# Kernel tuning notes

Hardware: AMD Instinct MI355X
Metric: run time of the kernel (lower is better)

The kernel has to match this reference:

```python
import jax, jax.numpy as jnp
import numpy as np

B, H, W = 2, 56, 56
D_MODEL, D_STATE, D_CONV, DT_RANK, K = 96, 16, 3, 6, 4
D_INNER = 192  # expand=2.0 * d_model


def _hscan1(x):
    # torch get_horizontal_scan1: flip odd columns along H; involution. x: (B,C,H,W)
    cols = (jnp.arange(x.shape[3]) % 2) == 1
    return jnp.where(cols[None, None, None, :], x[:, :, ::-1, :], x)


def _vscan1(x):
    # torch get_vertical_scan1: flip odd rows along W, then transpose H<->W. (B,C,H,W)->(B,C,W,H)
    rows = (jnp.arange(x.shape[2]) % 2) == 1
    x = jnp.where(rows[None, None, :, None], x[:, :, :, ::-1], x)
    return jnp.swapaxes(x, 2, 3)


def _revert_vscan1(x):
    # inverse of _vscan1. x: (B,C,W,H) -> (B,C,H,W)
    x = jnp.swapaxes(x, 2, 3)
    rows = (jnp.arange(x.shape[2]) % 2) == 1
    return jnp.where(rows[None, None, :, None], x[:, :, :, ::-1], x)


def _selective_scan(u, delta, A, Bs, Cs, D, delta_bias):
    # u, delta: (B, K*d, L); A: (K*d, N); Bs, Cs: (B, K, N, L); D: (K*d,)
    Bb, KD, L = u.shape
    k = Bs.shape[1]
    d = KD // k
    N = A.shape[1]
    delta = jax.nn.softplus(delta + delta_bias[None, :, None])
    u4 = u.reshape(Bb, k, d, L)
    dt4 = delta.reshape(Bb, k, d, L)
    A4 = A.reshape(k, d, N)
    dA = jnp.exp(jnp.einsum('bkdl,kdn->lbkdn', dt4, A4))           # (L,B,K,d,N)
    dBu = jnp.einsum('bkdl,bknl,bkdl->lbkdn', dt4, Bs, u4)          # (L,B,K,d,N)
    Ct = jnp.transpose(Cs, (3, 0, 1, 2))                            # (L,B,K,N)
    h0 = jnp.zeros((Bb, k, d, N), u.dtype)

    def step(h, inp):
        dA_t, dBu_t, C_t = inp
        h = dA_t * h + dBu_t
        y = jnp.einsum('bkdn,bkn->bkd', h, C_t)
        return h, y

    _, ys = jax.lax.scan(step, h0, (dA, dBu, Ct))                   # ys: (L,B,K,d)
    y = jnp.transpose(ys, (1, 2, 3, 0)).reshape(Bb, KD, L)
    return y + u * D[None, :, None]


def reference(x, in_proj_w, conv_w, conv_b, x_proj_weight, dt_projs_weight,
              dt_projs_bias, A_logs, Ds, out_norm_w, out_norm_b, out_proj_w):
    Bb, Hh, Ww, _ = x.shape
    L = Hh * Ww
    xz = jnp.einsum('bhwc,ec->bhwe', x, in_proj_w)
    xc, z = jnp.split(xz, 2, axis=-1)
    xc = jnp.transpose(xc, (0, 3, 1, 2))                            # (B, d_inner, H, W)
    xc = jax.lax.conv_general_dilated(xc, conv_w, (1, 1), ((1, 1), (1, 1)),
                                      feature_group_count=D_INNER)
    xc = jax.nn.silu(xc + conv_b[None, :, None, None])
    # torch code mutates x in place: vertical scan sees the h-scanned tensor
    x1 = _hscan1(xc)
    x_hw = x1.reshape(Bb, 1, D_INNER, L)
    x2 = _vscan1(x1)
    x_wh = x2.reshape(Bb, 1, D_INNER, L)
    xs = jnp.concatenate([x_hw, x_wh, x_hw[..., ::-1], x_wh[..., ::-1]], axis=1)  # (B,K,d,L)
    x_dbl = jnp.einsum('bkdl,kcd->bkcl', xs, x_proj_weight)
    dts, Bs, Cs = jnp.split(x_dbl, [DT_RANK, DT_RANK + D_STATE], axis=2)
    dts = jnp.einsum('bkrl,kdr->bkdl', dts, dt_projs_weight)
    u = xs.reshape(Bb, K * D_INNER, L)
    delta = dts.reshape(Bb, K * D_INNER, L)
    A = -jnp.exp(A_logs)
    out_y = _selective_scan(u, delta, A, Bs, Cs, Ds, dt_projs_bias.reshape(-1))
    oy = out_y.reshape(Bb, K, D_INNER, L)
    # revert scans back to a common spatial layout and sum
    s0 = _hscan1(oy[:, 0].reshape(Bb, D_INNER, Hh, Ww))
    s2 = _hscan1(oy[:, 2, :, ::-1].reshape(Bb, D_INNER, Hh, Ww))
    s1 = _hscan1(_revert_vscan1(oy[:, 1].reshape(Bb, D_INNER, Ww, Hh)))
    s3 = _hscan1(_revert_vscan1(oy[:, 3, :, ::-1].reshape(Bb, D_INNER, Ww, Hh)))
    y = (s0 + s1 + s2 + s3).reshape(Bb, D_INNER, L)
    y = jnp.transpose(y, (0, 2, 1))                                 # (B, L, d_inner)
    mu = jnp.mean(y, axis=-1, keepdims=True)
    var = jnp.var(y, axis=-1, keepdims=True)
    y = (y - mu) / jnp.sqrt(var + 1e-5) * out_norm_w + out_norm_b
    y = y.reshape(Bb, Hh, Ww, D_INNER) * jax.nn.silu(z)
    return jnp.einsum('bhwd,cd->bhwc', y, out_proj_w)


def setup_inputs():
    key = jax.random.key(0)
    ks = jax.random.split(key, 8)
    s = 0.02
    return {
        "x": jax.random.normal(ks[0], (B, H, W, D_MODEL), jnp.float32),
        "in_proj_w": jax.random.normal(ks[1], (2 * D_INNER, D_MODEL), jnp.float32) * s,
        "conv_w": jax.random.normal(ks[2], (D_INNER, 1, D_CONV, D_CONV), jnp.float32) * s,
        "conv_b": jnp.zeros((D_INNER,), jnp.float32),
        "x_proj_weight": jax.random.normal(ks[3], (K, DT_RANK + 2 * D_STATE, D_INNER), jnp.float32) * s,
        "dt_projs_weight": jax.random.normal(ks[4], (K, D_INNER, DT_RANK), jnp.float32) * (DT_RANK ** -0.5),
        "dt_projs_bias": jax.random.uniform(ks[5], (K, D_INNER), jnp.float32, -4.6, -2.3),
        "A_logs": jnp.log(jnp.tile(jnp.arange(1, D_STATE + 1, dtype=jnp.float32)[None, :], (K * D_INNER, 1))),
        "Ds": jnp.ones((K * D_INNER,), jnp.float32),
        "out_norm_w": jnp.ones((D_INNER,), jnp.float32),
        "out_norm_b": jnp.zeros((D_INNER,), jnp.float32),
        "out_proj_w": jax.random.normal(ks[6], (D_MODEL, D_INNER), jnp.float32) * s,
    }
```

## Files before the change

kernel.cpp:

```cpp
#include <hip/hip_runtime.h>
#include <hip/hip_bf16.h>

#define BB 2
#define HH 56
#define WW 56
#define LL (HH*WW)
#define DM 96
#define DI 192
#define NS 16
#define DTR 6
#define KK 4
#define CDBL (DTR + 2*NS)
#define CS 32
#define NC 98
#define ROWS (BB*KK*DI)

#define IP_BM 32
__global__ __launch_bounds__(256) void k_inproj(const float* __restrict__ x,
                                                const float* __restrict__ w,
                                                float* __restrict__ xcpre,
                                                float* __restrict__ zsilu) {
    __shared__ float xl[IP_BM*100];
    __shared__ float wl[64*100];
    int t = threadIdx.x;
    int bl0 = blockIdx.x * IP_BM;
    for (int idx = t; idx < IP_BM*96; idx += 256) {
        int r = idx/96, c = idx%96;
        xl[r*100+c] = x[(bl0+r)*DM + c];
    }
    int pg = t >> 4, eg = t & 15;
    for (int nc = 0; nc < 6; ++nc) {
        __syncthreads();
        for (int idx = t; idx < 64*96; idx += 256) {
            int r = idx/96, c = idx%96;
            wl[r*100+c] = w[(nc*64+r)*DM + c];
        }
        __syncthreads();
        float acc[2][4] = {};
        #pragma unroll 4
        for (int k = 0; k < 96; ++k) {
            float a0 = xl[(pg*2+0)*100+k];
            float a1 = xl[(pg*2+1)*100+k];
            float b0 = wl[(eg*4+0)*100+k];
            float b1 = wl[(eg*4+1)*100+k];
            float b2 = wl[(eg*4+2)*100+k];
            float b3 = wl[(eg*4+3)*100+k];
            acc[0][0] = fmaf(a0,b0,acc[0][0]); acc[0][1] = fmaf(a0,b1,acc[0][1]);
            acc[0][2] = fmaf(a0,b2,acc[0][2]); acc[0][3] = fmaf(a0,b3,acc[0][3]);
            acc[1][0] = fmaf(a1,b0,acc[1][0]); acc[1][1] = fmaf(a1,b1,acc[1][1]);
            acc[1][2] = fmaf(a1,b2,acc[1][2]); acc[1][3] = fmaf(a1,b3,acc[1][3]);
        }
        #pragma unroll
        for (int j = 0; j < 2; ++j) {
            int bl = bl0 + pg*2 + j;
            #pragma unroll
            for (int jj = 0; jj < 4; ++jj) {
                int e = nc*64 + eg*4 + jj;
                float v = acc[j][jj];
                if (e < DI) xcpre[(size_t)bl*DI + e] = v;
                else        zsilu[(size_t)bl*DI + (e-DI)] = v / (1.f + expf(-v));
            }
        }
    }
}

__global__ __launch_bounds__(DI) void k_conv(const float* __restrict__ xcpre,
                                             const float* __restrict__ cw,
                                             const float* __restrict__ cb,
                                             float* __restrict__ xs0,
                                             float* __restrict__ xs1) {
    int bl = blockIdx.x;
    int b = bl / LL, l = bl % LL;
    int h = l / WW, w = l % WW;
    int c = threadIdx.x;
    float acc = cb[c];
    #pragma unroll
    for (int dh = -1; dh <= 1; ++dh) {
        int hh = h + dh;
        if (hh < 0 || hh >= HH) continue;
        #pragma unroll
        for (int dw = -1; dw <= 1; ++dw) {
            int ww2 = w + dw;
            if (ww2 < 0 || ww2 >= WW) continue;
            acc = fmaf(xcpre[(b*LL + hh*WW + ww2)*DI + c],
                       cw[c*9 + (dh+1)*3 + (dw+1)], acc);
        }
    }
    float v = acc / (1.f + expf(-acc));
    int i  = (w & 1) ? (HH-1-h) : h;
    int l0 = i*WW + w;
    int l1 = ((i & 1) ? (WW-1-w) : w)*HH + i;
    xs0[(b*LL + l0)*DI + c] = v;
    xs1[(b*LL + l1)*DI + c] = v;
}

#define TL 32
#define KCH 48
#define NKC 4
#define XSTR 52
#define WSTR 52
__global__ __launch_bounds__(256) void k_proj(const float* __restrict__ xs0,
                                              const float* __restrict__ xs1,
                                              const float* __restrict__ xpw,
                                              const float* __restrict__ dtw,
                                              const float* __restrict__ dtb,
                                              float* __restrict__ delta,
                                              float* __restrict__ Bsb,
                                              float* __restrict__ Csb) {
    int tile = blockIdx.x, k = blockIdx.y, b = blockIdx.z;
    int bk = b*KK + k;
    int t = threadIdx.x;
    __shared__ float Xl[TL*XSTR];
    __shared__ float Wl[39*WSTR];
    __shared__ float dblL[DTR*36];

    const float* src = (k & 1) ? xs1 : xs0;
    const bool rev = (k >= 2);
    int cp = t >> 4, lp = t & 15;

    float acc[3][2] = {};
    for (int kc = 0; kc < NKC; ++kc) {
        __syncthreads();
        for (int idx = t; idx < 39*12; idx += 256) {
            int r = idx/12, q = idx%12;
            float4 v = (r < CDBL)
                ? ((const float4*)(xpw + (size_t)k*CDBL*DI + (size_t)r*DI + kc*KCH))[q]
                : make_float4(0.f,0.f,0.f,0.f);
            *(float4*)&Wl[r*WSTR + 4*q] = v;
        }
        for (int idx = t; idx < TL*12; idx += 256) {
            int ll = idx/12, q = idx%12;
            int lg = tile*TL + ll;
            int lpos = rev ? (LL-1-lg) : lg;
            *(float4*)&Xl[ll*XSTR + 4*q] =
                ((const float4*)(src + (size_t)(b*LL + lpos)*DI + kc*KCH))[q];
        }
        __syncthreads();
        if (cp < 13) {
            const float4* w0 = (const float4*)&Wl[(3*cp+0)*WSTR];
            const float4* w1 = (const float4*)&Wl[(3*cp+1)*WSTR];
            const float4* w2 = (const float4*)&Wl[(3*cp+2)*WSTR];
            const float4* x0 = (const float4*)&Xl[(lp    )*XSTR];
            const float4* x1 = (const float4*)&Xl[(lp+16)*XSTR];
            #pragma unroll
            for (int q = 0; q < 12; ++q) {
                float4 wa = w0[q], wb = w1[q], wc = w2[q];
                float4 xa = x0[q], xb = x1[q];
                acc[0][0]=fmaf(wa.x,xa.x,acc[0][0]); acc[0][0]=fmaf(wa.y,xa.y,acc[0][0]);
                acc[0][0]=fmaf(wa.z,xa.z,acc[0][0]); acc[0][0]=fmaf(wa.w,xa.w,acc[0][0]);
                acc[0][1]=fmaf(wa.x,xb.x,acc[0][1]); acc[0][1]=fmaf(wa.y,xb.y,acc[0][1]);
                acc[0][1]=fmaf(wa.z,xb.z,acc[0][1]); acc[0][1]=fmaf(wa.w,xb.w,acc[0][1]);
                acc[1][0]=fmaf(wb.x,xa.x,acc[1][0]); acc[1][0]=fmaf(wb.y,xa.y,acc[1][0]);
                acc[1][0]=fmaf(wb.z,xa.z,acc[1][0]); acc[1][0]=fmaf(wb.w,xa.w,acc[1][0]);
                acc[1][1]=fmaf(wb.x,xb.x,acc[1][1]); acc[1][1]=fmaf(wb.y,xb.y,acc[1][1]);
                acc[1][1]=fmaf(wb.z,xb.z,acc[1][1]); acc[1][1]=fmaf(wb.w,xb.w,acc[1][1]);
                acc[2][0]=fmaf(wc.x,xa.x,acc[2][0]); acc[2][0]=fmaf(wc.y,xa.y,acc[2][0]);
                acc[2][0]=fmaf(wc.z,xa.z,acc[2][0]); acc[2][0]=fmaf(wc.w,xa.w,acc[2][0]);
                acc[2][1]=fmaf(wc.x,xb.x,acc[2][1]); acc[2][1]=fmaf(wc.y,xb.y,acc[2][1]);
                acc[2][1]=fmaf(wc.z,xb.z,acc[2][1]); acc[2][1]=fmaf(wc.w,xb.w,acc[2][1]);
            }
        }
    }
    if (cp < 13) {
        #pragma unroll
        for (int ci = 0; ci < 3; ++ci) {
            int c = 3*cp + ci;
            if (c < CDBL) {
                #pragma unroll
                for (int li = 0; li < 2; ++li) {
                    int ll = lp + 16*li;
                    int lg = tile*TL + ll;
                    float v = acc[ci][li];
                    if (c < DTR)          dblL[c*36 + ll] = v;
                    else if (c < DTR+NS)  Bsb[((size_t)bk*LL + lg)*NS + (c-DTR)] = v;
                    else                  Csb[((size_t)bk*LL + lg)*NS + (c-DTR-NS)] = v;
                }
            }
        }
    }
    __syncthreads();

    float wr0[DTR], wr1[DTR], wr2[DTR], bb0, bb1, bb2;
    {
        int d0 = t % DI, d1 = (t+64) % DI, d2 = (t+128) % DI;
        #pragma unroll
        for (int r = 0; r < DTR; ++r) {
            wr0[r] = dtw[((size_t)k*DI + d0)*DTR + r];
            wr1[r] = dtw[((size_t)k*DI + d1)*DTR + r];
            wr2[r] = dtw[((size_t)k*DI + d2)*DTR + r];
        }
        bb0 = dtb[k*DI + d0]; bb1 = dtb[k*DI + d1]; bb2 = dtb[k*DI + d2];
    }
    float* dbase = delta + ((size_t)bk*LL + (size_t)tile*TL)*DI;
    for (int j3 = 0; j3 < 8; ++j3) {
        #pragma unroll
        for (int jj = 0; jj < 3; ++jj) {
            int j = j3*3 + jj;
            int idx = t + 256*j;
            int d = idx % DI;
            int ll = idx / DI;
            float a = (jj == 0) ? bb0 : (jj == 1) ? bb1 : bb2;
            const float* wrp = (jj == 0) ? wr0 : (jj == 1) ? wr1 : wr2;
            #pragma unroll
            for (int r = 0; r < DTR; ++r) a = fmaf(wrp[r], dblL[r*36 + ll], a);
            float sp = fmaxf(a, 0.f) + log1pf(expf(-fabsf(a)));
            dbase[(size_t)ll*DI + d] = sp;
        }
    }
}

__global__ __launch_bounds__(192) void k_scan1(const float* __restrict__ delta,
                                               const float* __restrict__ xs0,
                                               const float* __restrict__ xs1,
                                               const float* __restrict__ Bsb,
                                               const float* __restrict__ A_logs,
                                               float* __restrict__ P,
                                               float* __restrict__ Hend) {
    int c = blockIdx.x, bk = blockIdx.y;
    int k = bk & 3, b = bk >> 2;
    int d = threadIdx.x;
    int kd = k*DI + d;
    __shared__ float Bl[CS*NS];
    const float* bsrc = Bsb + ((size_t)bk*LL + c*CS)*NS;
    for (int i = threadIdx.x; i < CS*NS/4; i += 192)
        ((float4*)Bl)[i] = ((const float4*)bsrc)[i];

    float A[NS], h[NS], p[NS];
    #pragma unroll
    for (int q = 0; q < 4; ++q) {
        float4 av = *(const float4*)&A_logs[kd*NS + 4*q];
        A[4*q+0] = -expf(av.x); A[4*q+1] = -expf(av.y);
        A[4*q+2] = -expf(av.z); A[4*q+3] = -expf(av.w);
    }
    #pragma unroll
    for (int n = 0; n < NS; ++n) { h[n] = 0.f; p[n] = 1.f; }
    __syncthreads();

    const bool rev = (k >= 2);
    const float* dp = delta + ((size_t)bk*LL + c*CS)*DI + d;
    const float* up = ((k & 1) ? xs1 : xs0) + (size_t)b*LL*DI + d;
    const int l0 = c*CS;

    #pragma unroll 2
    for (int i = 0; i < CS; ++i) {
        float dt = dp[(size_t)i*DI];
        int lp = rev ? (LL-1-(l0+i)) : (l0+i);
        float u = up[(size_t)lp*DI];
        float dtu = dt * u;
        float Bv[NS];
        #pragma unroll
        for (int q = 0; q < 4; ++q)
            *(float4*)&Bv[4*q] = *(const float4*)&Bl[i*NS + 4*q];
        #pragma unroll
        for (int n = 0; n < NS; ++n) {
            float dA = __expf(dt * A[n]);
            h[n] = fmaf(dA, h[n], dtu * Bv[n]);
            p[n] *= dA;
        }
    }
    size_t obase = ((size_t)c*ROWS + bk*DI + d)*NS;
    #pragma unroll
    for (int q = 0; q < 4; ++q) {
        *(float4*)&P[obase + 4*q]    = make_float4(p[4*q], p[4*q+1], p[4*q+2], p[4*q+3]);
        *(float4*)&Hend[obase + 4*q] = make_float4(h[4*q], h[4*q+1], h[4*q+2], h[4*q+3]);
    }
}

__global__ __launch_bounds__(256) void k_scanmid(const float* __restrict__ P,
                                                 const float* __restrict__ Hend,
                                                 float* __restrict__ Hin) {
    int tid = blockIdx.x*256 + threadIdx.x;
    float h = 0.f;
    for (int c = 0; c < NC; ++c) {
        size_t idx = (size_t)c*(ROWS*NS) + tid;
        Hin[idx] = h;
        h = fmaf(P[idx], h, Hend[idx]);
    }
}

__global__ __launch_bounds__(192) void k_scan2(const float* __restrict__ delta,
                                               const float* __restrict__ xs0,
                                               const float* __restrict__ xs1,
                                               const float* __restrict__ Bsb,
                                               const float* __restrict__ Csb,
                                               const float* __restrict__ A_logs,
                                               const float* __restrict__ Ds,
                                               const float* __restrict__ Hin,
                                               float* __restrict__ oy) {
    int c = blockIdx.x, bk = blockIdx.y;
    int k = bk & 3, b = bk >> 2;
    int d = threadIdx.x;
    int kd = k*DI + d;
    __shared__ float Bl[CS*NS];
    __shared__ float Cl[CS*NS];
    const float* bsrc = Bsb + ((size_t)bk*LL + c*CS)*NS;
    const float* csrc = Csb + ((size_t)bk*LL + c*CS)*NS;
    for (int i = threadIdx.x; i < CS*NS/4; i += 192) {
        ((float4*)Bl)[i] = ((const float4*)bsrc)[i];
        ((float4*)Cl)[i] = ((const float4*)csrc)[i];
    }

    float A[NS], h[NS];
    #pragma unroll
    for (int q = 0; q < 4; ++q) {
        float4 av = *(const float4*)&A_logs[kd*NS + 4*q];
        A[4*q+0] = -expf(av.x); A[4*q+1] = -expf(av.y);
        A[4*q+2] = -expf(av.z); A[4*q+3] = -expf(av.w);
    }
    size_t ibase = ((size_t)c*ROWS + bk*DI + d)*NS;
    #pragma unroll
    for (int q = 0; q < 4; ++q) {
        float4 hv = *(const float4*)&Hin[ibase + 4*q];
        h[4*q+0] = hv.x; h[4*q+1] = hv.y; h[4*q+2] = hv.z; h[4*q+3] = hv.w;
    }
    const float Dv = Ds[kd];
    __syncthreads();

    const bool rev = (k >= 2);
    const float* dp = delta + ((size_t)bk*LL + c*CS)*DI + d;
    const float* up = ((k & 1) ? xs1 : xs0) + (size_t)b*LL*DI + d;
    float* yp = oy + ((size_t)bk*LL + c*CS)*DI + d;
    const int l0 = c*CS;

    #pragma unroll 2
    for (int i = 0; i < CS; ++i) {
        float dt = dp[(size_t)i*DI];
        int lp = rev ? (LL-1-(l0+i)) : (l0+i);
        float u = up[(size_t)lp*DI];
        float dtu = dt * u;
        float Bv[NS], Cv[NS];
        #pragma unroll
        for (int q = 0; q < 4; ++q) {
            *(float4*)&Bv[4*q] = *(const float4*)&Bl[i*NS + 4*q];
            *(float4*)&Cv[4*q] = *(const float4*)&Cl[i*NS + 4*q];
        }
        float acc = 0.f;
        #pragma unroll
        for (int n = 0; n < NS; ++n) {
            float dA = __expf(dt * A[n]);
            h[n] = fmaf(dA, h[n], dtu * Bv[n]);
            acc = fmaf(h[n], Cv[n], acc);
        }
        yp[(size_t)i*DI] = fmaf(u, Dv, acc);
    }
}

#define OP_BM 32
__global__ __launch_bounds__(256) void k_out(const float* __restrict__ oy,
                                             const float* __restrict__ zsilu,
                                             const float* __restrict__ onw,
                                             const float* __restrict__ onb,
                                             const float* __restrict__ opw,
                                             float* __restrict__ out) {
    __shared__ float yv[OP_BM*196];
    __shared__ float wl[96*68];
    int t = threadIdx.x;
    int bl0 = blockIdx.x * OP_BM;
    int lane = t & 63, wv = t >> 6;

    for (int pp = 0; pp < 8; ++pp) {
        int p = wv*8 + pp;
        int bl = bl0 + p;
        int b = bl / LL, l = bl % LL;
        int h = l / WW, w2 = l % WW;
        int i = (w2 & 1) ? (HH-1-h) : h;
        int l0 = i*WW + w2;
        int l1 = ((i & 1) ? (WW-1-w2) : w2)*HH + i;
        size_t base = (size_t)b*KK*LL*DI;
        float yd[3]; float s1 = 0.f, s2 = 0.f;
        #pragma unroll
        for (int j = 0; j < 3; ++j) {
            int c = lane + j*64;
            float v = oy[base + (size_t)(0*LL + l0)*DI + c]
                    + oy[base + (size_t)(1*LL + l1)*DI + c]
                    + oy[base + (size_t)(2*LL + (LL-1-l0))*DI + c]
                    + oy[base + (size_t)(3*LL + (LL-1-l1))*DI + c];
            yd[j] = v; s1 += v; s2 += v*v;
        }
        #pragma unroll
        for (int m = 1; m < 64; m <<= 1) { s1 += __shfl_xor(s1, m); s2 += __shfl_xor(s2, m); }
        float mu  = s1 / DI;
        float var = s2 / DI - mu*mu;
        float ry  = rsqrtf(var + 1e-5f);
        #pragma unroll
        for (int j = 0; j < 3; ++j) {
            int c = lane + j*64;
            float yn = (yd[j] - mu) * ry * onw[c] + onb[c];
            yv[p*196 + c] = yn * zsilu[(size_t)bl*DI + c];
        }
    }

    int pg = t >> 5, eg = t & 31;
    float acc[4][3] = {};
    for (int kc = 0; kc < 3; ++kc) {
        __syncthreads();
        for (int idx = t; idx < 96*64; idx += 256) {
            int r = idx >> 6, c = idx & 63;
            wl[r*68 + c] = opw[r*DI + kc*64 + c];
        }
        __syncthreads();
        #pragma unroll 4
        for (int kk = 0; kk < 64; ++kk) {
            float a[4], bq[3];
            #pragma unroll
            for (int j = 0; j < 4; ++j)  a[j]  = yv[(pg*4+j)*196 + kc*64 + kk];
            #pragma unroll
            for (int jj = 0; jj < 3; ++jj) bq[jj] = wl[(eg*3+jj)*68 + kk];
            #pragma unroll
            for (int j = 0; j < 4; ++j)
                #pragma unroll
                for (int jj = 0; jj < 3; ++jj)
                    acc[j][jj] = fmaf(a[j], bq[jj], acc[j][jj]);
        }
    }
    #pragma unroll
    for (int j = 0; j < 4; ++j) {
        int bl = bl0 + pg*4 + j;
        #pragma unroll
        for (int jj = 0; jj < 3; ++jj)
            out[(size_t)bl*DM + eg*3 + jj] = acc[j][jj];
    }
}

extern "C" void kernel_launch(void* const* d_in, const int* in_sizes, int n_in,
                              void* d_out, int out_size, void* d_ws, size_t ws_size,
                              hipStream_t stream) {
    const float* x      = (const float*)d_in[0];
    const float* ipw    = (const float*)d_in[1];
    const float* convw  = (const float*)d_in[2];
    const float* convb  = (const float*)d_in[3];
    const float* xpw    = (const float*)d_in[4];
    const float* dtw    = (const float*)d_in[5];
    const float* dtb    = (const float*)d_in[6];
    const float* A_logs = (const float*)d_in[7];
    const float* Ds     = (const float*)d_in[8];
    const float* onw    = (const float*)d_in[9];
    const float* onb    = (const float*)d_in[10];
    const float* opw    = (const float*)d_in[11];
    float* out = (float*)d_out;

    float* ws = (float*)d_ws;
    const size_t SZ_BLD  = (size_t)BB*LL*DI;
    const size_t SZ_BKLD = (size_t)BB*KK*LL*DI;
    const size_t SZ_BKLN = (size_t)BB*KK*LL*NS;
    const size_t SZ_ST   = (size_t)NC*ROWS*NS;
    float* xcpre = ws;
    float* zsilu = xcpre + SZ_BLD;
    float* xs0   = zsilu + SZ_BLD;
    float* xs1   = xs0   + SZ_BLD;
    float* delta = xs1   + SZ_BLD;
    float* Bsb   = delta + SZ_BKLD;
    float* Csb   = Bsb   + SZ_BKLN;
    float* oy    = Csb   + SZ_BKLN;
    float* Hin   = oy    + SZ_BKLD;
    float* Hend  = oy;
    float* P     = oy + SZ_ST;

    k_inproj<<<(BB*LL)/IP_BM, 256, 0, stream>>>(x, ipw, xcpre, zsilu);
    k_conv<<<BB*LL, DI, 0, stream>>>(xcpre, convw, convb, xs0, xs1);
    dim3 g3(LL/TL, KK, BB);
    k_proj<<<g3, 256, 0, stream>>>(xs0, xs1, xpw, dtw, dtb, delta, Bsb, Csb);
    dim3 gs(NC, BB*KK);
    k_scan1<<<gs, 192, 0, stream>>>(delta, xs0, xs1, Bsb, A_logs, P, Hend);
    k_scanmid<<<(ROWS*NS)/256, 256, 0, stream>>>(P, Hend, Hin);
    k_scan2<<<gs, 192, 0, stream>>>(delta, xs0, xs1, Bsb, Csb, A_logs, Ds, Hin, oy);
    k_out<<<(BB*LL)/OP_BM, 256, 0, stream>>>(oy, zsilu, onw, onb, opw, out);
}
```

Measured before the change: 259.1 us.

## Vectorize shared-memory GEMM loads, flatten conv indexing, restructure delta softplus

The in_proj and out_proj GEMM inner loops now read float4 vectors from LDS, and the in_proj weight rows are permuted so each thread reads contiguous rows. Global-to-LDS staging uses float4 loads without per-element div/mod. The depthwise conv uses a 3D grid with explicit neighbour offsets and fast __expf. In k_proj, each of 192 threads now computes delta for one channel across all 32 positions, using fast exp/log intrinsics. Together these aim to cut integer index arithmetic and LDS instruction count, at some cost in accuracy from the fast math and extra register pressure in the delta loop.

```diff
diff --git a/kernel.cpp b/kernel.cpp
--- a/kernel.cpp
+++ b/kernel.cpp
@@ -24,31 +24,45 @@
     __shared__ float wl[64*100];
     int t = threadIdx.x;
     int bl0 = blockIdx.x * IP_BM;
-    for (int idx = t; idx < IP_BM*96; idx += 256) {
-        int r = idx/96, c = idx%96;
-        xl[r*100+c] = x[(bl0+r)*DM + c];
-    }
+    int qs = t & 31;
+    for (int r = t >> 5; r < IP_BM; r += 8)
+        if (qs < 24)
+            *(float4*)&xl[r*100 + 4*qs] = *(const float4*)&x[(size_t)(bl0+r)*DM + 4*qs];
     int pg = t >> 4, eg = t & 15;
     for (int nc = 0; nc < 6; ++nc) {
         __syncthreads();
-        for (int idx = t; idx < 64*96; idx += 256) {
-            int r = idx/96, c = idx%96;
-            wl[r*100+c] = w[(nc*64+r)*DM + c];
-        }
+        for (int r = t >> 5; r < 64; r += 8)
+            if (qs < 24)
+                *(float4*)&wl[((r&3)*16 + (r>>2))*100 + 4*qs] =
+                    *(const float4*)&w[(size_t)(nc*64+r)*DM + 4*qs];
         __syncthreads();
         float acc[2][4] = {};
-        #pragma unroll 4
-        for (int k = 0; k < 96; ++k) {
-            float a0 = xl[(pg*2+0)*100+k];
-            float a1 = xl[(pg*2+1)*100+k];
-            float b0 = wl[(eg*4+0)*100+k];
-            float b1 = wl[(eg*4+1)*100+k];
-            float b2 = wl[(eg*4+2)*100+k];
-            float b3 = wl[(eg*4+3)*100+k];
-            acc[0][0] = fmaf(a0,b0,acc[0][0]); acc[0][1] = fmaf(a0,b1,acc[0][1]);
-            acc[0][2] = fmaf(a0,b2,acc[0][2]); acc[0][3] = fmaf(a0,b3,acc[0][3]);
-            acc[1][0] = fmaf(a1,b0,acc[1][0]); acc[1][1] = fmaf(a1,b1,acc[1][1]);
-            acc[1][2] = fmaf(a1,b2,acc[1][2]); acc[1][3] = fmaf(a1,b3,acc[1][3]);
+        const float4* xa4 = (const float4*)&xl[(pg*2+0)*100];
+        const float4* xb4 = (const float4*)&xl[(pg*2+1)*100];
+        const float4* w0 = (const float4*)&wl[(0*16+eg)*100];
+        const float4* w1 = (const float4*)&wl[(1*16+eg)*100];
+        const float4* w2 = (const float4*)&wl[(2*16+eg)*100];
+        const float4* w3 = (const float4*)&wl[(3*16+eg)*100];
+        #pragma unroll 6
+        for (int q = 0; q < 24; ++q) {
+            float4 xa = xa4[q], xb = xb4[q];
+            float4 b0 = w0[q], b1 = w1[q], b2 = w2[q], b3 = w3[q];
+            acc[0][0]=fmaf(xa.x,b0.x,acc[0][0]); acc[0][0]=fmaf(xa.y,b0.y,acc[0][0]);
+            acc[0][0]=fmaf(xa.z,b0.z,acc[0][0]); acc[0][0]=fmaf(xa.w,b0.w,acc[0][0]);
+            acc[0][1]=fmaf(xa.x,b1.x,acc[0][1]); acc[0][1]=fmaf(xa.y,b1.y,acc[0][1]);
+            acc[0][1]=fmaf(xa.z,b1.z,acc[0][1]); acc[0][1]=fmaf(xa.w,b1.w,acc[0][1]);
+            acc[0][2]=fmaf(xa.x,b2.x,acc[0][2]); acc[0][2]=fmaf(xa.y,b2.y,acc[0][2]);
+            acc[0][2]=fmaf(xa.z,b2.z,acc[0][2]); acc[0][2]=fmaf(xa.w,b2.w,acc[0][2]);
+            acc[0][3]=fmaf(xa.x,b3.x,acc[0][3]); acc[0][3]=fmaf(xa.y,b3.y,acc[0][3]);
+            acc[0][3]=fmaf(xa.z,b3.z,acc[0][3]); acc[0][3]=fmaf(xa.w,b3.w,acc[0][3]);
+            acc[1][0]=fmaf(xb.x,b0.x,acc[1][0]); acc[1][0]=fmaf(xb.y,b0.y,acc[1][0]);
+            acc[1][0]=fmaf(xb.z,b0.z,acc[1][0]); acc[1][0]=fmaf(xb.w,b0.w,acc[1][0]);
+            acc[1][1]=fmaf(xb.x,b1.x,acc[1][1]); acc[1][1]=fmaf(xb.y,b1.y,acc[1][1]);
+            acc[1][1]=fmaf(xb.z,b1.z,acc[1][1]); acc[1][1]=fmaf(xb.w,b1.w,acc[1][1]);
+            acc[1][2]=fmaf(xb.x,b2.x,acc[1][2]); acc[1][2]=fmaf(xb.y,b2.y,acc[1][2]);
+            acc[1][2]=fmaf(xb.z,b2.z,acc[1][2]); acc[1][2]=fmaf(xb.w,b2.w,acc[1][2]);
+            acc[1][3]=fmaf(xb.x,b3.x,acc[1][3]); acc[1][3]=fmaf(xb.y,b3.y,acc[1][3]);
+            acc[1][3]=fmaf(xb.z,b3.z,acc[1][3]); acc[1][3]=fmaf(xb.w,b3.w,acc[1][3]);
         }
         #pragma unroll
         for (int j = 0; j < 2; ++j) {
@@ -58,7 +72,7 @@
                 int e = nc*64 + eg*4 + jj;
                 float v = acc[j][jj];
                 if (e < DI) xcpre[(size_t)bl*DI + e] = v;
-                else        zsilu[(size_t)bl*DI + (e-DI)] = v / (1.f + expf(-v));
+                else        zsilu[(size_t)bl*DI + (e-DI)] = v / (1.f + __expf(-v));
             }
         }
     }
@@ -69,36 +83,38 @@
                                              const float* __restrict__ cb,
                                              float* __restrict__ xs0,
                                              float* __restrict__ xs1) {
-    int bl = blockIdx.x;
-    int b = bl / LL, l = bl % LL;
-    int h = l / WW, w = l % WW;
+    int w = blockIdx.x, h = blockIdx.y, b = blockIdx.z;
     int c = threadIdx.x;
+    const float* src = xcpre + ((size_t)(b*LL + h*WW + w))*DI + c;
+    const float* cwc = cw + c*9;
     float acc = cb[c];
-    #pragma unroll
-    for (int dh = -1; dh <= 1; ++dh) {
-        int hh = h + dh;
-        if (hh < 0 || hh >= HH) continue;
-        #pragma unroll
-        for (int dw = -1; dw <= 1; ++dw) {
-            int ww2 = w + dw;
-            if (ww2 < 0 || ww2 >= WW) continue;
-            acc = fmaf(xcpre[(b*LL + hh*WW + ww2)*DI + c],
-                       cw[c*9 + (dh+1)*3 + (dw+1)], acc);
-        }
-    }
-    float v = acc / (1.f + expf(-acc));
+    if (h > 0) {
+        if (w > 0)      acc = fmaf(src[-(WW+1)*DI], cwc[0], acc);
+                        acc = fmaf(src[-WW*DI],     cwc[1], acc);
+        if (w < WW-1)   acc = fmaf(src[-(WW-1)*DI], cwc[2], acc);
+    }
+    {
+        if (w > 0)      acc = fmaf(src[-DI],        cwc[3], acc);
+                        acc = fmaf(src[0],          cwc[4], acc);
+        if (w < WW-1)   acc = fmaf(src[DI],         cwc[5], acc);
+    }
+    if (h < HH-1) {
+        if (w > 0)      acc = fmaf(src[(WW-1)*DI],  cwc[6], acc);
+                        acc = fmaf(src[WW*DI],      cwc[7], acc);
+        if (w < WW-1)   acc = fmaf(src[(WW+1)*DI],  cwc[8], acc);
+    }
+    float v = acc / (1.f + __expf(-acc));
     int i  = (w & 1) ? (HH-1-h) : h;
     int l0 = i*WW + w;
     int l1 = ((i & 1) ? (WW-1-w) : w)*HH + i;
-    xs0[(b*LL + l0)*DI + c] = v;
-    xs1[(b*LL + l1)*DI + c] = v;
+    xs0[((size_t)b*LL + l0)*DI + c] = v;
+    xs1[((size_t)b*LL + l1)*DI + c] = v;
 }
 
 #define TL 32
 #define KCH 48
 #define NKC 4
-#define XSTR 52
-#define WSTR 52
+#define LSTR 52
 __global__ __launch_bounds__(256) void k_proj(const float* __restrict__ xs0,
                                               const float* __restrict__ xs1,
                                               const float* __restrict__ xpw,
@@ -110,38 +126,39 @@
     int tile = blockIdx.x, k = blockIdx.y, b = blockIdx.z;
     int bk = b*KK + k;
     int t = threadIdx.x;
-    __shared__ float Xl[TL*XSTR];
-    __shared__ float Wl[39*WSTR];
+    __shared__ float Xl[TL*LSTR];
+    __shared__ float Wl[39*LSTR];
     __shared__ float dblL[DTR*36];
 
     const float* src = (k & 1) ? xs1 : xs0;
     const bool rev = (k >= 2);
     int cp = t >> 4, lp = t & 15;
+    int qs = t & 15;
 
     float acc[3][2] = {};
     for (int kc = 0; kc < NKC; ++kc) {
         __syncthreads();
-        for (int idx = t; idx < 39*12; idx += 256) {
-            int r = idx/12, q = idx%12;
-            float4 v = (r < CDBL)
-                ? ((const float4*)(xpw + (size_t)k*CDBL*DI + (size_t)r*DI + kc*KCH))[q]
-                : make_float4(0.f,0.f,0.f,0.f);
-            *(float4*)&Wl[r*WSTR + 4*q] = v;
-        }
-        for (int idx = t; idx < TL*12; idx += 256) {
-            int ll = idx/12, q = idx%12;
-            int lg = tile*TL + ll;
-            int lpos = rev ? (LL-1-lg) : lg;
-            *(float4*)&Xl[ll*XSTR + 4*q] =
-                ((const float4*)(src + (size_t)(b*LL + lpos)*DI + kc*KCH))[q];
-        }
+        for (int r = t >> 4; r < 39; r += 16)
+            if (qs < 12) {
+                float4 v = (r < CDBL)
+                    ? *(const float4*)&xpw[(size_t)k*CDBL*DI + (size_t)r*DI + kc*KCH + 4*qs]
+                    : make_float4(0.f,0.f,0.f,0.f);
+                *(float4*)&Wl[r*LSTR + 4*qs] = v;
+            }
+        for (int r = t >> 4; r < TL; r += 16)
+            if (qs < 12) {
+                int lg = tile*TL + r;
+                int lpos = rev ? (LL-1-lg) : lg;
+                *(float4*)&Xl[r*LSTR + 4*qs] =
+                    *(const float4*)&src[(size_t)(b*LL + lpos)*DI + kc*KCH + 4*qs];
+            }
         __syncthreads();
         if (cp < 13) {
-            const float4* w0 = (const float4*)&Wl[(3*cp+0)*WSTR];
-            const float4* w1 = (const float4*)&Wl[(3*cp+1)*WSTR];
-            const float4* w2 = (const float4*)&Wl[(3*cp+2)*WSTR];
-            const float4* x0 = (const float4*)&Xl[(lp    )*XSTR];
-            const float4* x1 = (const float4*)&Xl[(lp+16)*XSTR];
+            const float4* w0 = (const float4*)&Wl[(3*cp+0)*LSTR];
+            const float4* w1 = (const float4*)&Wl[(3*cp+1)*LSTR];
+            const float4* w2 = (const float4*)&Wl[(3*cp+2)*LSTR];
+            const float4* x0 = (const float4*)&Xl[(lp    )*LSTR];
+            const float4* x1 = (const float4*)&Xl[(lp+16)*LSTR];
             #pragma unroll
             for (int q = 0; q < 12; ++q) {
                 float4 wa = w0[q], wb = w1[q], wc = w2[q];
@@ -180,31 +197,34 @@
     }
     __syncthreads();
 
-    float wr0[DTR], wr1[DTR], wr2[DTR], bb0, bb1, bb2;
-    {
-        int d0 = t % DI, d1 = (t+64) % DI, d2 = (t+128) % DI;
+    if (t < DI) {
+        int d = t;
+        float wr[DTR];
+        #pragma unroll
+        for (int r = 0; r < DTR; ++r) wr[r] = dtw[((size_t)k*DI + d)*DTR + r];
+        float bias = dtb[k*DI + d];
+        float a2[TL];
+        #pragma unroll
+        for (int ll = 0; ll < TL; ++ll) a2[ll] = bias;
         #pragma unroll
         for (int r = 0; r < DTR; ++r) {
-            wr0[r] = dtw[((size_t)k*DI + d0)*DTR + r];
-            wr1[r] = dtw[((size_t)k*DI + d1)*DTR + r];
-            wr2[r] = dtw[((size_t)k*DI + d2)*DTR + r];
-        }
-        bb0 = dtb[k*DI + d0]; bb1 = dtb[k*DI + d1]; bb2 = dtb[k*DI + d2];
-    }
-    float* dbase = delta + ((size_t)bk*LL + (size_t)tile*TL)*DI;
-    for (int j3 = 0; j3 < 8; ++j3) {
-        #pragma unroll
-        for (int jj = 0; jj < 3; ++jj) {
-            int j = j3*3 + jj;
-            int idx = t + 256*j;
-            int d = idx % DI;
-            int ll = idx / DI;
-            float a = (jj == 0) ? bb0 : (jj == 1) ? bb1 : bb2;
-            const float* wrp = (jj == 0) ? wr0 : (jj == 1) ? wr1 : wr2;
+            float wv = wr[r];
+            const float4* db = (const float4*)&dblL[r*36];
             #pragma unroll
-            for (int r = 0; r < DTR; ++r) a = fmaf(wrp[r], dblL[r*36 + ll], a);
-            float sp = fmaxf(a, 0.f) + log1pf(expf(-fabsf(a)));
-            dbase[(size_t)ll*DI + d] = sp;
+            for (int q = 0; q < 8; ++q) {
+                float4 v = db[q];
+                a2[4*q+0] = fmaf(wv, v.x, a2[4*q+0]);
+                a2[4*q+1] = fmaf(wv, v.y, a2[4*q+1]);
+                a2[4*q+2] = fmaf(wv, v.z, a2[4*q+2]);
+                a2[4*q+3] = fmaf(wv, v.w, a2[4*q+3]);
+            }
+        }
+        float* dst = delta + ((size_t)bk*LL + (size_t)tile*TL)*DI + d;
+        #pragma unroll
+        for (int ll = 0; ll < TL; ++ll) {
+            float a = a2[ll];
+            float sp = fmaxf(a, 0.f) + __logf(1.f + __expf(-fabsf(a)));
+            dst[ll*DI] = sp;
         }
     }
 }
@@ -356,12 +376,13 @@
     __shared__ float wl[96*68];
     int t = threadIdx.x;
     int bl0 = blockIdx.x * OP_BM;
+    int b = (blockIdx.x >= (LL/OP_BM)) ? 1 : 0;
+    int lbase = bl0 - b*LL;
     int lane = t & 63, wv = t >> 6;
 
     for (int pp = 0; pp < 8; ++pp) {
         int p = wv*8 + pp;
-        int bl = bl0 + p;
-        int b = bl / LL, l = bl % LL;
+        int l = lbase + p;
         int h = l / WW, w2 = l % WW;
         int i = (w2 & 1) ? (HH-1-h) : h;
         int l0 = i*WW + w2;
@@ -386,7 +407,7 @@
         for (int j = 0; j < 3; ++j) {
             int c = lane + j*64;
             float yn = (yd[j] - mu) * ry * onw[c] + onb[c];
-            yv[p*196 + c] = yn * zsilu[(size_t)bl*DI + c];
+            yv[p*196 + c] = yn * zsilu[(size_t)(bl0+p)*DI + c];
         }
     }
 
@@ -394,23 +415,45 @@
     float acc[4][3] = {};
     for (int kc = 0; kc < 3; ++kc) {
         __syncthreads();
-        for (int idx = t; idx < 96*64; idx += 256) {
-            int r = idx >> 6, c = idx & 63;
-            wl[r*68 + c] = opw[r*DI + kc*64 + c];
-        }
+        for (int r = t >> 4; r < 96; r += 16)
+            *(float4*)&wl[r*68 + 4*(t&15)] =
+                *(const float4*)&opw[(size_t)r*DI + kc*64 + 4*(t&15)];
         __syncthreads();
-        #pragma unroll 4
-        for (int kk = 0; kk < 64; ++kk) {
-            float a[4], bq[3];
-            #pragma unroll
-            for (int j = 0; j < 4; ++j)  a[j]  = yv[(pg*4+j)*196 + kc*64 + kk];
-            #pragma unroll
-            for (int jj = 0; jj < 3; ++jj) bq[jj] = wl[(eg*3+jj)*68 + kk];
-            #pragma unroll
-            for (int j = 0; j < 4; ++j)
-                #pragma unroll
-                for (int jj = 0; jj < 3; ++jj)
-                    acc[j][jj] = fmaf(a[j], bq[jj], acc[j][jj]);
+        const float4* y0 = (const float4*)&yv[(pg*4+0)*196 + kc*64];
+        const float4* y1 = (const float4*)&yv[(pg*4+1)*196 + kc*64];
+        const float4* y2 = (const float4*)&yv[(pg*4+2)*196 + kc*64];
+        const float4* y3 = (const float4*)&yv[(pg*4+3)*196 + kc*64];
+        const float4* w0 = (const float4*)&wl[(eg*3+0)*68];
+        const float4* w1 = (const float4*)&wl[(eg*3+1)*68];
+        const float4* w2 = (const float4*)&wl[(eg*3+2)*68];
+        #pragma unroll
+        for (int q = 0; q < 16; ++q) {
+            float4 a0 = y0[q], a1 = y1[q], a2 = y2[q], a3 = y3[q];
+            float4 b0 = w0[q], b1 = w1[q], b2 = w2[q];
+            acc[0][0]=fmaf(a0.x,b0.x,acc[0][0]); acc[0][0]=fmaf(a0.y,b0.y,acc[0][0]);
+            acc[0][0]=fmaf(a0.z,b0.z,acc[0][0]); acc[0][0]=fmaf(a0.w,b0.w,acc[0][0]);
+            acc[0][1]=fmaf(a0.x,b1.x,acc[0][1]); acc[0][1]=fmaf(a0.y,b1.y,acc[0][1]);
+            acc[0][1]=fmaf(a0.z,b1.z,acc[0][1]); acc[0][1]=fmaf(a0.w,b1.w,acc[0][1]);
+            acc[0][2]=fmaf(a0.x,b2.x,acc[0][2]); acc[0][2]=fmaf(a0.y,b2.y,acc[0][2]);
+            acc[0][2]=fmaf(a0.z,b2.z,acc[0][2]); acc[0][2]=fmaf(a0.w,b2.w,acc[0][2]);
+            acc[1][0]=fmaf(a1.x,b0.x,acc[1][0]); acc[1][0]=fmaf(a1.y,b0.y,acc[1][0]);
+            acc[1][0]=fmaf(a1.z,b0.z,acc[1][0]); acc[1][0]=fmaf(a1.w,b0.w,acc[1][0]);
+            acc[1][1]=fmaf(a1.x,b1.x,acc[1][1]); acc[1][1]=fmaf(a1.y,b1.y,acc[1][1]);
+            acc[1][1]=fmaf(a1.z,b1.z,acc[1][1]); acc[1][1]=fmaf(a1.w,b1.w,acc[1][1]);
+            acc[1][2]=fmaf(a1.x,b2.x,acc[1][2]); acc[1][2]=fmaf(a1.y,b2.y,acc[1][2]);
+            acc[1][2]=fmaf(a1.z,b2.z,acc[1][2]); acc[1][2]=fmaf(a1.w,b2.w,acc[1][2]);
+            acc[2][0]=fmaf(a2.x,b0.x,acc[2][0]); acc[2][0]=fmaf(a2.y,b0.y,acc[2][0]);
+            acc[2][0]=fmaf(a2.z,b0.z,acc[2][0]); acc[2][0]=fmaf(a2.w,b0.w,acc[2][0]);
+            acc[2][1]=fmaf(a2.x,b1.x,acc[2][1]); acc[2][1]=fmaf(a2.y,b1.y,acc[2][1]);
+            acc[2][1]=fmaf(a2.z,b1.z,acc[2][1]); acc[2][1]=fmaf(a2.w,b1.w,acc[2][1]);
+            acc[2][2]=fmaf(a2.x,b2.x,acc[2][2]); acc[2][2]=fmaf(a2.y,b2.y,acc[2][2]);
+            acc[2][2]=fmaf(a2.z,b2.z,acc[2][2]); acc[2][2]=fmaf(a2.w,b2.w,acc[2][2]);
+            acc[3][0]=fmaf(a3.x,b0.x,acc[3][0]); acc[3][0]=fmaf(a3.y,b0.y,acc[3][0]);
+            acc[3][0]=fmaf(a3.z,b0.z,acc[3][0]); acc[3][0]=fmaf(a3.w,b0.w,acc[3][0]);
+            acc[3][1]=fmaf(a3.x,b1.x,acc[3][1]); acc[3][1]=fmaf(a3.y,b1.y,acc[3][1]);
+            acc[3][1]=fmaf(a3.z,b1.z,acc[3][1]); acc[3][1]=fmaf(a3.w,b1.w,acc[3][1]);
+            acc[3][2]=fmaf(a3.x,b2.x,acc[3][2]); acc[3][2]=fmaf(a3.y,b2.y,acc[3][2]);
+            acc[3][2]=fmaf(a3.z,b2.z,acc[3][2]); acc[3][2]=fmaf(a3.w,b2.w,acc[3][2]);
         }
     }
     #pragma unroll
@@ -457,7 +500,7 @@
     float* P     = oy + SZ_ST;
 
     k_inproj<<<(BB*LL)/IP_BM, 256, 0, stream>>>(x, ipw, xcpre, zsilu);
-    k_conv<<<BB*LL, DI, 0, stream>>>(xcpre, convw, convb, xs0, xs1);
+    k_conv<<<dim3(WW, HH, BB), DI, 0, stream>>>(xcpre, convw, convb, xs0, xs1);
     dim3 g3(LL/TL, KK, BB);
     k_proj<<<g3, 256, 0, stream>>>(xs0, xs1, xpw, dtw, dtb, delta, Bsb, Csb);
     dim3 gs(NC, BB*KK);
```

Measured after the change: 244.5 us. 5.7% less time.
